# Performance work log

Hardware: AMD Instinct MI355X
Metric: run time of the kernel (lower is better)

Reference implementation:

```python
import jax, jax.numpy as jnp
import numpy as np

B, S, E = 4, 2048, 1024
H = 16
D = E // H  # head_dim = 64


def setup_inputs() -> dict:
    key = jax.random.key(0)
    k1, k2, k3 = jax.random.split(key, 3)
    x = jax.random.normal(k1, (B, S, E), dtype=jnp.float32)
    w_qkv = jax.random.normal(k2, (E, 3 * E), dtype=jnp.float32) * (E ** -0.5)
    b_qkv = jnp.zeros((3 * E,), dtype=jnp.float32)
    w_proj = jax.random.normal(k3, (E, E), dtype=jnp.float32) * (E ** -0.5)
    b_proj = jnp.zeros((E,), dtype=jnp.float32)
    return {"x": x, "w_qkv": w_qkv, "b_qkv": b_qkv, "w_proj": w_proj, "b_proj": b_proj}


def reference(x, w_qkv, b_qkv, w_proj, b_proj):
    bsz, seq_len, emb = x.shape
    scale = D ** -0.5
    qkv = x @ w_qkv + b_qkv                      # [B,S,3E]
    q, k, v = jnp.split(qkv, 3, axis=2)
    # [B,S,E] -> [B,H,S,D]
    q = q.reshape(bsz, seq_len, H, D).transpose(0, 2, 1, 3)
    k = k.reshape(bsz, seq_len, H, D).transpose(0, 2, 1, 3)
    v = v.reshape(bsz, seq_len, H, D).transpose(0, 2, 1, 3)
    att = jnp.einsum('bhqd,bhkd->bhqk', q, k) * scale
    causal = jnp.tril(jnp.ones((seq_len, seq_len), dtype=bool))
    att = jnp.where(causal, att, -jnp.inf)
    att = jax.nn.softmax(att, axis=-1)
    y = jnp.einsum('bhqk,bhkd->bhqd', att, v)
    y = y.transpose(0, 2, 1, 3).reshape(bsz, seq_len, emb)
    return y @ w_proj + b_proj
```

## Files before the change

kernel.cpp:

```cpp
#include <hip/hip_runtime.h>
#include <hip/hip_bf16.h>
#include <stdint.h>

#define S_LEN 2048
#define EMB   1024
#define NH    16
#define HD    64

typedef unsigned short u16;
typedef __attribute__((ext_vector_type(4))) float f32x4;
typedef __attribute__((ext_vector_type(8))) short bf16x8;

typedef __attribute__((address_space(1))) const unsigned char gas_t;
typedef __attribute__((address_space(3))) unsigned char las_t;

static __device__ __forceinline__ void gld_lds16(const void* g, void* l) {
  __builtin_amdgcn_global_load_lds((gas_t*)g, (las_t*)l, 16, 0, 0);
}

static __device__ __forceinline__ u16 f2bf(float f) {
  unsigned int u = __builtin_bit_cast(unsigned int, f);
  u = u + 0x7fffu + ((u >> 16) & 1u);
  return (u16)(u >> 16);
}

static __device__ __forceinline__ float fexp2(float x) {
  float r;
  asm("v_exp_f32 %0, %1" : "=v"(r) : "v"(x));
  return r;
}

static __device__ __forceinline__ unsigned cvt_pk_bf16(float lo, float hi) {
  unsigned r;
  asm("v_cvt_pk_bf16_f32 %0, %1, %2" : "=v"(r) : "v"(lo), "v"(hi));
  return r;
}

static __device__ __forceinline__ float red4rows_max(float x) {
  unsigned u = __builtin_bit_cast(unsigned, x);
  auto r = __builtin_amdgcn_permlane32_swap(u, u, false, false);
  float y = fmaxf(__builtin_bit_cast(float, (unsigned)r[0]),
                  __builtin_bit_cast(float, (unsigned)r[1]));
  unsigned v = __builtin_bit_cast(unsigned, y);
  auto r2 = __builtin_amdgcn_permlane16_swap(v, v, false, false);
  return fmaxf(__builtin_bit_cast(float, (unsigned)r2[0]),
               __builtin_bit_cast(float, (unsigned)r2[1]));
}
static __device__ __forceinline__ float red4rows_sum(float x) {
  unsigned u = __builtin_bit_cast(unsigned, x);
  auto r = __builtin_amdgcn_permlane32_swap(u, u, false, false);
  float y = __builtin_bit_cast(float, (unsigned)r[0]) +
            __builtin_bit_cast(float, (unsigned)r[1]);
  unsigned v = __builtin_bit_cast(unsigned, y);
  auto r2 = __builtin_amdgcn_permlane16_swap(v, v, false, false);
  return __builtin_bit_cast(float, (unsigned)r2[0]) +
         __builtin_bit_cast(float, (unsigned)r2[1]);
}

__global__ __launch_bounds__(256) void k_cvt(const float* __restrict__ in,
                                             u16* __restrict__ out, int n4) {
  int i = blockIdx.x * blockDim.x + threadIdx.x;
  int stride = gridDim.x * blockDim.x;
  for (; i < n4; i += stride) {
    float4 f = ((const float4*)in)[i];
    ushort4 o;
    o.x = f2bf(f.x); o.y = f2bf(f.y); o.z = f2bf(f.z); o.w = f2bf(f.w);
    ((ushort4*)out)[i] = o;
  }
}

__global__ __launch_bounds__(256) void k_transpose_cvt(const float* __restrict__ W,
                                                       u16* __restrict__ WT,
                                                       int K, int N) {
  __shared__ u16 tile[64][68];
  const int c0 = blockIdx.x * 64, r0 = blockIdx.y * 64;
  const int t = threadIdx.x;
  const int tr = t >> 4, tc4 = (t & 15) * 4;
#pragma unroll
  for (int i = 0; i < 4; i++) {
    const int r = tr + 16 * i;
    float4 f = *(const float4*)&W[(size_t)(r0 + r) * N + c0 + tc4];
    ushort4 o;
    o.x = f2bf(f.x); o.y = f2bf(f.y); o.z = f2bf(f.z); o.w = f2bf(f.w);
    *(ushort4*)&tile[r][tc4] = o;
  }
  __syncthreads();
  const int oc = t >> 2, or0 = (t & 3) * 16;
  u16 vals[16];
#pragma unroll
  for (int j = 0; j < 16; j++) vals[j] = tile[or0 + j][oc];
  u16* dst = &WT[(size_t)(c0 + oc) * K + r0 + or0];
  *(uint4*)dst = *(const uint4*)&vals[0];
  *(uint4*)(dst + 8) = *(const uint4*)&vals[8];
}

template <int MODE>
__global__ __launch_bounds__(256) void k_gemm(const u16* __restrict__ A,
                                              const u16* __restrict__ BT,
                                              const float* __restrict__ bias,
                                              float* __restrict__ Cout,
                                              u16* __restrict__ q_ws,
                                              u16* __restrict__ k_ws,
                                              u16* __restrict__ v_t,
                                              int N, int K) {
  __shared__ u16 As[2][128 * 32];
  __shared__ u16 Bs[2][128 * 32];
  const int tid = threadIdx.x;
  const int w = tid >> 6, lane = tid & 63;
  const int wr = w >> 1, wc = w & 1;
  const int lrow = lane & 15, lk8 = (lane >> 4) * 8;
  const int brow = blockIdx.y * 128, bcol = blockIdx.x * 128;
  const int srow = lane >> 2;
  const int scol = (lane & 3) * 8;

  const f32x4 zero = {0.f, 0.f, 0.f, 0.f};
  f32x4 acc[4][4];
#pragma unroll
  for (int m = 0; m < 4; m++)
#pragma unroll
    for (int n = 0; n < 4; n++) acc[m][n] = zero;

  auto stage = [&](int kt, int buf) {
#pragma unroll
    for (int i = 0; i < 2; i++) {
      const int c = w * 2 + i;
      const int row = c * 16 + srow;
      gld_lds16(&A[(size_t)(brow + row) * K + kt + scol], (void*)(&As[buf][c * 512]));
      gld_lds16(&BT[(size_t)(bcol + row) * K + kt + scol], (void*)(&Bs[buf][c * 512]));
    }
  };

  const int NK = K >> 5;
  stage(0, 0);
  __syncthreads();
  for (int it = 0; it < NK; ++it) {
    const int cur = it & 1;
    if (it + 1 < NK) stage((it + 1) << 5, cur ^ 1);
    bf16x8 af[4], bfr[4];
#pragma unroll
    for (int mt = 0; mt < 4; mt++)
      af[mt] = *(const bf16x8*)&As[cur][(wr * 64 + mt * 16 + lrow) * 32 + lk8];
#pragma unroll
    for (int nt = 0; nt < 4; nt++)
      bfr[nt] = *(const bf16x8*)&Bs[cur][(wc * 64 + nt * 16 + lrow) * 32 + lk8];
    __builtin_amdgcn_s_setprio(1);
#pragma unroll
    for (int mt = 0; mt < 4; mt++)
#pragma unroll
      for (int nt = 0; nt < 4; nt++)
        acc[mt][nt] = __builtin_amdgcn_mfma_f32_16x16x32_bf16(af[mt], bfr[nt],
                                                              acc[mt][nt], 0, 0, 0);
    __builtin_amdgcn_s_setprio(0);
    __syncthreads();
  }

  if constexpr (MODE == 0) {
    const int which = bcol >> 10;
#pragma unroll
    for (int mt = 0; mt < 4; mt++)
#pragma unroll
      for (int nt = 0; nt < 4; nt++) {
        const int col = bcol + wc * 64 + nt * 16 + lrow;
        const int e = col & 1023;
        const int h = e >> 6, d = e & 63;
        const int row0 = brow + wr * 64 + mt * 16 + (lane >> 4) * 4;
        const int b = row0 >> 11, s0 = row0 & 2047;
        const size_t bh = (size_t)(b * NH + h);
        const float bv = bias[col];
        if (which == 2) {
          ushort4 pk;
          pk.x = f2bf(acc[mt][nt][0] + bv);
          pk.y = f2bf(acc[mt][nt][1] + bv);
          pk.z = f2bf(acc[mt][nt][2] + bv);
          pk.w = f2bf(acc[mt][nt][3] + bv);
          *(ushort4*)&v_t[(bh * HD + d) * S_LEN + s0] = pk;
        } else {
          u16* dst = which ? k_ws : q_ws;
#pragma unroll
          for (int r = 0; r < 4; r++)
            dst[(bh * S_LEN + s0 + r) * HD + d] = f2bf(acc[mt][nt][r] + bv);
        }
      }
  } else {
#pragma unroll
    for (int mt = 0; mt < 4; mt++)
#pragma unroll
      for (int nt = 0; nt < 4; nt++)
#pragma unroll
        for (int r = 0; r < 4; r++) {
          const int row = brow + wr * 64 + mt * 16 + (lane >> 4) * 4 + r;
          const int col = bcol + wc * 64 + nt * 16 + lrow;
          Cout[(size_t)row * N + col] = acc[mt][nt][r] + bias[col];
        }
  }
}

__global__ __launch_bounds__(256, 2) void k_attn(const u16* __restrict__ q_ws,
                                                 const u16* __restrict__ k_ws,
                                                 const u16* __restrict__ v_t,
                                                 u16* __restrict__ y) {
  __shared__ u16 Kl[2][64 * 64];
  __shared__ u16 Vl[2][64 * 64];
  const int tid = threadIdx.x;
  const int w = tid >> 6, lane = tid & 63;
  const int lrow = lane & 15, lk8 = (lane >> 4) * 8;
  const int g4 = (lane >> 4) * 4;
  const int pr = blockIdx.x;
  const int tileA = pr, tileB = 31 - pr;
  const int bh = blockIdx.y;
  const size_t base = (size_t)bh * S_LEN * HD;
  const float SC = 0.125f * 1.4426950408889634f;

  bf16x8 qfA[2], qfB[2];
#pragma unroll
  for (int ks = 0; ks < 2; ks++) {
    qfA[ks] = *(const bf16x8*)&q_ws[base + (size_t)(tileA * 64 + w * 16 + lrow) * HD + ks * 32 + lk8];
    qfB[ks] = *(const bf16x8*)&q_ws[base + (size_t)(tileB * 64 + w * 16 + lrow) * HD + ks * 32 + lk8];
  }

  const f32x4 zero = {0.f, 0.f, 0.f, 0.f};
  f32x4 oA[4], oB[4];
#pragma unroll
  for (int dt = 0; dt < 4; dt++) { oA[dt] = zero; oB[dt] = zero; }
  float mA = -1e30f, lA = 0.f, mB = -1e30f, lB = 0.f;

  auto stage = [&](int jb, int buf) {
#pragma unroll
    for (int i = 0; i < 2; i++) {
      const int c = w * 2 + i;
      const int row = c * 8 + (lane >> 3);
      const int blk = (lane & 7) ^ (row & 7);
      gld_lds16(&k_ws[base + (size_t)(jb * 64 + row) * HD + blk * 8],
                (void*)(&Kl[buf][c * 512]));
      gld_lds16(&v_t[base + (size_t)row * S_LEN + jb * 64 + blk * 8],
                (void*)(&Vl[buf][c * 512]));
    }
  };

  auto process = [&](int cur, const bf16x8 (&kf)[2][4], const bf16x8 (&qf)[2],
                     f32x4 (&o)[4], float& m_run, float& l_run, bool maskDiag) {
    f32x4 sa[4];
#pragma unroll
    for (int nt = 0; nt < 4; nt++) sa[nt] = zero;
    __builtin_amdgcn_s_setprio(1);
#pragma unroll
    for (int ks = 0; ks < 2; ks++)
#pragma unroll
      for (int nt = 0; nt < 4; nt++)
        sa[nt] = __builtin_amdgcn_mfma_f32_16x16x32_bf16(kf[ks][nt], qf[ks], sa[nt], 0, 0, 0);
    __builtin_amdgcn_s_setprio(0);

    float sv[4][4];
#pragma unroll
    for (int nt = 0; nt < 4; nt++)
#pragma unroll
      for (int r = 0; r < 4; r++) {
        float x = sa[nt][r] * SC;
        if (maskDiag && (nt * 16 + g4 + r) > (w * 16 + lrow)) x = -3.0e38f;
        sv[nt][r] = x;
      }

    float mx = fmaxf(fmaxf(fmaxf(sv[0][0], sv[0][1]), fmaxf(sv[0][2], sv[0][3])),
                     fmaxf(fmaxf(sv[1][0], sv[1][1]), fmaxf(sv[1][2], sv[1][3])));
    mx = fmaxf(mx,
               fmaxf(fmaxf(fmaxf(sv[2][0], sv[2][1]), fmaxf(sv[2][2], sv[2][3])),
                     fmaxf(fmaxf(sv[3][0], sv[3][1]), fmaxf(sv[3][2], sv[3][3]))));
    mx = red4rows_max(mx);
    const float mn = fmaxf(m_run, mx);
    const float alpha = fexp2(m_run - mn);
    float sum = 0.f;
#pragma unroll
    for (int nt = 0; nt < 4; nt++)
#pragma unroll
      for (int r = 0; r < 4; r++) {
        const float p = fexp2(sv[nt][r] - mn);
        sv[nt][r] = p;
        sum += p;
      }
    sum = red4rows_sum(sum);
    l_run = l_run * alpha + sum;
    m_run = mn;
#pragma unroll
    for (int dt = 0; dt < 4; dt++) o[dt] *= alpha;

    unsigned pk[4][2];
#pragma unroll
    for (int nt = 0; nt < 4; nt++) {
      pk[nt][0] = cvt_pk_bf16(sv[nt][0], sv[nt][1]);
      pk[nt][1] = cvt_pk_bf16(sv[nt][2], sv[nt][3]);
    }
    union { unsigned u[4]; bf16x8 v; } c0, c1;
    {
      auto r0 = __builtin_amdgcn_permlane32_swap(pk[0][0], pk[1][0], false, false);
      auto s0 = __builtin_amdgcn_permlane16_swap(r0[0], r0[1], false, false);
      auto r1 = __builtin_amdgcn_permlane32_swap(pk[0][1], pk[1][1], false, false);
      auto s1 = __builtin_amdgcn_permlane16_swap(r1[0], r1[1], false, false);
      c0.u[0] = s0[0]; c0.u[1] = s1[0]; c0.u[2] = s0[1]; c0.u[3] = s1[1];
      auto r2 = __builtin_amdgcn_permlane32_swap(pk[2][0], pk[3][0], false, false);
      auto s2 = __builtin_amdgcn_permlane16_swap(r2[0], r2[1], false, false);
      auto r3 = __builtin_amdgcn_permlane32_swap(pk[2][1], pk[3][1], false, false);
      auto s3 = __builtin_amdgcn_permlane16_swap(r3[0], r3[1], false, false);
      c1.u[0] = s2[0]; c1.u[1] = s3[0]; c1.u[2] = s2[1]; c1.u[3] = s3[1];
    }
    bf16x8 pfrag[2] = {c0.v, c1.v};

    __builtin_amdgcn_s_setprio(1);
#pragma unroll
    for (int ks = 0; ks < 2; ks++)
#pragma unroll
      for (int dt = 0; dt < 4; dt++) {
        const int vr = dt * 16 + lrow;
        const int vblk = (ks * 4 + (lane >> 4)) ^ (vr & 7);
        bf16x8 vf = *(const bf16x8*)&Vl[cur][vr * 64 + vblk * 8];
        o[dt] = __builtin_amdgcn_mfma_f32_16x16x32_bf16(vf, pfrag[ks], o[dt], 0, 0, 0);
      }
    __builtin_amdgcn_s_setprio(0);
  };

  stage(0, 0);
  __syncthreads();
  for (int jb = 0; jb <= tileB; jb++) {
    const int cur = jb & 1;
    if (jb < tileB) stage(jb + 1, cur ^ 1);
    bf16x8 kf[2][4];
#pragma unroll
    for (int ks = 0; ks < 2; ks++)
#pragma unroll
      for (int nt = 0; nt < 4; nt++) {
        const int kvr = nt * 16 + lrow;
        const int blk = (ks * 4 + (lane >> 4)) ^ (kvr & 7);
        kf[ks][nt] = *(const bf16x8*)&Kl[cur][kvr * 64 + blk * 8];
      }
    process(cur, kf, qfB, oB, mB, lB, jb == tileB);
    if (jb <= tileA) process(cur, kf, qfA, oA, mA, lA, jb == tileA);
    __syncthreads();
  }

  const int b = bh >> 4, h = bh & 15;
  const float invA = 1.0f / lA;
  const float invB = 1.0f / lB;
  const int qgA = tileA * 64 + w * 16 + lrow;
  const int qgB = tileB * 64 + w * 16 + lrow;
#pragma unroll
  for (int dt = 0; dt < 4; dt++) {
    ushort4 sA, sB;
    sA.x = f2bf(oA[dt][0] * invA); sA.y = f2bf(oA[dt][1] * invA);
    sA.z = f2bf(oA[dt][2] * invA); sA.w = f2bf(oA[dt][3] * invA);
    sB.x = f2bf(oB[dt][0] * invB); sB.y = f2bf(oB[dt][1] * invB);
    sB.z = f2bf(oB[dt][2] * invB); sB.w = f2bf(oB[dt][3] * invB);
    *(ushort4*)&y[(size_t)(b * S_LEN + qgA) * EMB + h * HD + dt * 16 + g4] = sA;
    *(ushort4*)&y[(size_t)(b * S_LEN + qgB) * EMB + h * HD + dt * 16 + g4] = sB;
  }
}

extern "C" void kernel_launch(void* const* d_in, const int* in_sizes, int n_in,
                              void* d_out, int out_size, void* d_ws, size_t ws_size,
                              hipStream_t stream) {
  const float* x      = (const float*)d_in[0];
  const float* w_qkv  = (const float*)d_in[1];
  const float* b_qkv  = (const float*)d_in[2];
  const float* w_proj = (const float*)d_in[3];
  const float* b_proj = (const float*)d_in[4];
  float* out = (float*)d_out;

  char* ws = (char*)d_ws;
  u16* wqkvT  = (u16*)(ws);
  u16* wprojT = (u16*)(ws + 6291456);
  u16* xb     = (u16*)(ws + 8388608);
  u16* q_ws   = (u16*)(ws + 25165824);
  u16* k_ws   = (u16*)(ws + 41943040);
  u16* v_t    = (u16*)(ws + 58720256);
  u16* y_att  = xb;

  k_cvt<<<dim3(1024), dim3(256), 0, stream>>>(x, xb, (8192 * 1024) / 4);
  k_transpose_cvt<<<dim3(48, 16), dim3(256), 0, stream>>>(w_qkv, wqkvT, 1024, 3072);
  k_transpose_cvt<<<dim3(16, 16), dim3(256), 0, stream>>>(w_proj, wprojT, 1024, 1024);
  k_gemm<0><<<dim3(24, 64), dim3(256), 0, stream>>>(xb, wqkvT, b_qkv, nullptr,
                                                    q_ws, k_ws, v_t, 3072, 1024);
  k_attn<<<dim3(16, 64), dim3(256), 0, stream>>>(q_ws, k_ws, v_t, y_att);
  k_gemm<1><<<dim3(8, 64), dim3(256), 0, stream>>>(y_att, wprojT, b_proj, out,
                                                   nullptr, nullptr, nullptr, 1024, 1024);
}
```

Baseline: 201.9 us.

## Hoist V fragment loads, split mask path, skip rescale when max stays bounded

The V fragments are now loaded from LDS once per KV tile and shared by both query tiles, where before each query tile loaded them separately. The causal mask check moves to a separate branch so off-diagonal tiles avoid per-element compares. A lazy rescale skips the alpha exponential and the O/l rescaling when the wave-wide new max stays within 8 (log2 units) of the running max, as in FA4-style softmax. This adds register pressure from holding 8 extra bf16x8 V fragments, and lets the unnormalized exponentials grow up to 2^8.

```diff
diff --git a/kernel.cpp b/kernel.cpp
--- a/kernel.cpp
+++ b/kernel.cpp
@@ -237,8 +237,9 @@
     }
   };
 
-  auto process = [&](int cur, const bf16x8 (&kf)[2][4], const bf16x8 (&qf)[2],
-                     f32x4 (&o)[4], float& m_run, float& l_run, bool maskDiag) {
+  auto process = [&](const bf16x8 (&kf)[2][4], const bf16x8 (&vf)[2][4],
+                     const bf16x8 (&qf)[2], f32x4 (&o)[4], float& m_run,
+                     float& l_run, bool maskDiag) {
     f32x4 sa[4];
 #pragma unroll
     for (int nt = 0; nt < 4; nt++) sa[nt] = zero;
@@ -251,14 +252,21 @@
     __builtin_amdgcn_s_setprio(0);
 
     float sv[4][4];
-#pragma unroll
-    for (int nt = 0; nt < 4; nt++)
-#pragma unroll
-      for (int r = 0; r < 4; r++) {
-        float x = sa[nt][r] * SC;
-        if (maskDiag && (nt * 16 + g4 + r) > (w * 16 + lrow)) x = -3.0e38f;
-        sv[nt][r] = x;
-      }
+    if (maskDiag) {
+#pragma unroll
+      for (int nt = 0; nt < 4; nt++)
+#pragma unroll
+        for (int r = 0; r < 4; r++) {
+          float x = sa[nt][r] * SC;
+          if ((nt * 16 + g4 + r) > (w * 16 + lrow)) x = -3.0e38f;
+          sv[nt][r] = x;
+        }
+    } else {
+#pragma unroll
+      for (int nt = 0; nt < 4; nt++)
+#pragma unroll
+        for (int r = 0; r < 4; r++) sv[nt][r] = sa[nt][r] * SC;
+    }
 
     float mx = fmaxf(fmaxf(fmaxf(sv[0][0], sv[0][1]), fmaxf(sv[0][2], sv[0][3])),
                      fmaxf(fmaxf(sv[1][0], sv[1][1]), fmaxf(sv[1][2], sv[1][3])));
@@ -266,8 +274,16 @@
                fmaxf(fmaxf(fmaxf(sv[2][0], sv[2][1]), fmaxf(sv[2][2], sv[2][3])),
                      fmaxf(fmaxf(sv[3][0], sv[3][1]), fmaxf(sv[3][2], sv[3][3]))));
     mx = red4rows_max(mx);
-    const float mn = fmaxf(m_run, mx);
-    const float alpha = fexp2(m_run - mn);
+    const bool nogrow = __all(mx <= m_run + 8.0f);
+    float mn = m_run;
+    if (!nogrow) {
+      mn = fmaxf(m_run, mx);
+      const float alpha = fexp2(m_run - mn);
+      l_run *= alpha;
+#pragma unroll
+      for (int dt = 0; dt < 4; dt++) o[dt] *= alpha;
+      m_run = mn;
+    }
     float sum = 0.f;
 #pragma unroll
     for (int nt = 0; nt < 4; nt++)
@@ -278,10 +294,7 @@
         sum += p;
       }
     sum = red4rows_sum(sum);
-    l_run = l_run * alpha + sum;
-    m_run = mn;
-#pragma unroll
-    for (int dt = 0; dt < 4; dt++) o[dt] *= alpha;
+    l_run += sum;
 
     unsigned pk[4][2];
 #pragma unroll
@@ -308,12 +321,8 @@
 #pragma unroll
     for (int ks = 0; ks < 2; ks++)
 #pragma unroll
-      for (int dt = 0; dt < 4; dt++) {
-        const int vr = dt * 16 + lrow;
-        const int vblk = (ks * 4 + (lane >> 4)) ^ (vr & 7);
-        bf16x8 vf = *(const bf16x8*)&Vl[cur][vr * 64 + vblk * 8];
-        o[dt] = __builtin_amdgcn_mfma_f32_16x16x32_bf16(vf, pfrag[ks], o[dt], 0, 0, 0);
-      }
+      for (int dt = 0; dt < 4; dt++)
+        o[dt] = __builtin_amdgcn_mfma_f32_16x16x32_bf16(vf[ks][dt], pfrag[ks], o[dt], 0, 0, 0);
     __builtin_amdgcn_s_setprio(0);
   };
 
@@ -322,7 +331,7 @@
   for (int jb = 0; jb <= tileB; jb++) {
     const int cur = jb & 1;
     if (jb < tileB) stage(jb + 1, cur ^ 1);
-    bf16x8 kf[2][4];
+    bf16x8 kf[2][4], vf[2][4];
 #pragma unroll
     for (int ks = 0; ks < 2; ks++)
 #pragma unroll
@@ -330,9 +339,10 @@
         const int kvr = nt * 16 + lrow;
         const int blk = (ks * 4 + (lane >> 4)) ^ (kvr & 7);
         kf[ks][nt] = *(const bf16x8*)&Kl[cur][kvr * 64 + blk * 8];
+        vf[ks][nt] = *(const bf16x8*)&Vl[cur][kvr * 64 + blk * 8];
       }
-    process(cur, kf, qfB, oB, mB, lB, jb == tileB);
-    if (jb <= tileA) process(cur, kf, qfA, oA, mA, lA, jb == tileA);
+    process(kf, vf, qfB, oB, mB, lB, jb == tileB);
+    if (jb <= tileA) process(kf, vf, qfA, oA, mA, lA, jb == tileA);
     __syncthreads();
   }
 
```

Measured after the change: 197.5 us. 2.2% less time.
